# Optimization experiments

Measured on AMD Instinct MI355X. Metric: run time of the kernel, lower is better.

## Reference

```python
import jax, jax.numpy as jnp
import numpy as np

NQ = 6; DM = 128; CH = 4; SEQ = 2048; CHUNK = 16; BATCH = 128
NFP = 5 * NQ * 2   # feature params for 2 layers
NMP = 5 * NQ * 2   # mixing params for 2 layers

# ---- batched gate matrices (theta: (B,)) ----

def _rx(t):
    c = jnp.cos(t / 2).astype(jnp.complex64)
    s = (-1j * jnp.sin(t / 2)).astype(jnp.complex64)
    return jnp.stack([jnp.stack([c, s], -1), jnp.stack([s, c], -1)], -2)

def _ry(t):
    c = jnp.cos(t / 2).astype(jnp.complex64)
    s = jnp.sin(t / 2).astype(jnp.complex64)
    return jnp.stack([jnp.stack([c, -s], -1), jnp.stack([s, c], -1)], -2)

def _rz(t):
    e = jnp.exp(-1j * t.astype(jnp.complex64) / 2)
    z = jnp.zeros_like(e)
    return jnp.stack([jnp.stack([e, z], -1), jnp.stack([z, jnp.conj(e)], -1)], -2)

def _crx(t):
    B = t.shape[0]
    r = _rx(t)
    I = jnp.broadcast_to(jnp.eye(2, dtype=jnp.complex64), (B, 2, 2))
    Z = jnp.zeros((B, 2, 2), jnp.complex64)
    return jnp.concatenate([jnp.concatenate([I, Z], -1), jnp.concatenate([Z, r], -1)], -2)

# ---- batched statevector gate application; state: (B, 2, ..., 2) with axis 1+w = wire w ----

def _ap1(s, U, w):
    s = jnp.moveaxis(s, 1 + w, 1)
    sh = s.shape
    s = jnp.einsum('bij,bjr->bir', U, s.reshape(sh[0], 2, -1)).reshape(sh)
    return jnp.moveaxis(s, 1, 1 + w)

def _ap2(s, U, w0, w1):
    s = jnp.moveaxis(s, (1 + w0, 1 + w1), (1, 2))
    sh = s.shape
    s = jnp.einsum('bij,bjr->bir', U, s.reshape(sh[0], 4, -1)).reshape(sh)
    return jnp.moveaxis(s, (1, 2), (1 + w0, 1 + w1))

def _ansatz(s, p, off):
    # RX,RY,RZ on each qubit, then forward CRX ring, then backward CRX ring
    for i in range(NQ):
        s = _ap1(s, _rx(p[:, off + 3 * i]), i)
        s = _ap1(s, _ry(p[:, off + 3 * i + 1]), i)
        s = _ap1(s, _rz(p[:, off + 3 * i + 2]), i)
    off += 3 * NQ
    for i in range(NQ):
        s = _ap2(s, _crx(p[:, off]), i, (i + 1) % NQ)
        off += 1
    for i in range(NQ - 1, -1, -1):
        s = _ap2(s, _crx(p[:, off]), i, (i - 1) % NQ)
        off += 1
    return s, off

def _circuit(angles, fp, mp):
    B = angles.shape[0]
    s = jnp.zeros((B, 2 ** NQ), jnp.complex64).at[:, 0].set(1.0).reshape((B,) + (2,) * NQ)
    for i in range(NQ):                      # RY input embedding
        s = _ap1(s, _ry(angles[:, i]), i)
    off = 0
    for _ in range(2):                        # feature layers
        s, off = _ansatz(s, fp, off)
    off = 0
    for _ in range(2):                        # mixing layers
        s, off = _ansatz(s, mp, off)
    xs, ys, zs = [], [], []
    for i in range(NQ):                       # <X_i>, <Y_i>, <Z_i>
        v = jnp.moveaxis(s, 1 + i, 1).reshape(B, 2, -1)
        a, b = v[:, 0], v[:, 1]
        ab = jnp.sum(jnp.conj(a) * b, -1)
        xs.append(2 * jnp.real(ab))
        ys.append(2 * jnp.imag(ab))
        zs.append(jnp.sum(jnp.abs(a) ** 2 - jnp.abs(b) ** 2, -1))
    return jnp.stack(xs + ys + zs, 1)         # (B, 18) ordered X..Y..Z

def _ln(x, g, b, eps=1e-5):
    m = x.mean(-1, keepdims=True)
    v = ((x - m) ** 2).mean(-1, keepdims=True)
    return (x - m) / jnp.sqrt(v + eps) * g + b

def _fwd(x, conv_w, conv_b, ln1_g, ln1_b, ca1_w, ca1_b, ca2_w, ca2_b, pp_w, pp_b,
         ep_w, ep_b, op_w, op_b, ln2_g, ln2_b, sa1_w, sa1_b, sa2_w, sa2_b,
         cl1_w, cl1_b, cl2_w, cl2_b):
    B, C, S = x.shape
    h = jax.lax.conv_general_dilated(x, conv_w, (1,), [(1, 1)],
                                     dimension_numbers=('NCH', 'OIH', 'NCH')) + conv_b[None, :, None]
    h = jnp.transpose(h, (0, 2, 1))           # (B, S, D)
    h = _ln(h, ln1_g, ln1_b)
    nchunks = S // CHUNK
    h = h.reshape(B * nchunks, CHUNK, DM)
    sc = jnp.tanh(h @ ca1_w + ca1_b) @ ca2_w + ca2_b
    w = jax.nn.softmax(sc, axis=1)
    summ = jnp.sum(w * h, axis=1)             # (B*nchunks, D)
    ap = summ @ pp_w + pp_b
    fp, mp = ap[:, :NFP], ap[:, NFP:]
    ang = jnp.tanh(summ @ ep_w + ep_b) * np.pi
    q = _circuit(ang, fp, mp)                 # (B*nchunks, 18)
    cf = jax.nn.silu(_ln(q @ op_w + op_b, ln2_g, ln2_b))  # dropout = eval identity
    cf = cf.reshape(B, nchunks, DM)
    ss = jnp.tanh(cf @ sa1_w + sa1_b) @ sa2_w + sa2_b
    sw = jax.nn.softmax(ss, axis=1)
    rep = jnp.sum(sw * cf, axis=1)
    return jax.nn.silu(rep @ cl1_w + cl1_b) @ cl2_w + cl2_b

def setup_inputs() -> dict:
    key = jax.random.key(0)
    ks = jax.random.split(key, 16)
    n = lambda k, sh: (jax.random.normal(k, sh, jnp.float32) * 0.05)
    return {
        'x': jax.random.normal(ks[0], (BATCH, CH, SEQ), jnp.float32),
        'conv_w': n(ks[1], (DM, CH, 3)), 'conv_b': jnp.zeros((DM,), jnp.float32),
        'ln1_g': jnp.ones((DM,), jnp.float32), 'ln1_b': jnp.zeros((DM,), jnp.float32),
        'ca1_w': n(ks[2], (DM, DM // 4)), 'ca1_b': jnp.zeros((DM // 4,), jnp.float32),
        'ca2_w': n(ks[3], (DM // 4, 1)), 'ca2_b': jnp.zeros((1,), jnp.float32),
        'pp_w': n(ks[4], (DM, NFP + NMP)), 'pp_b': jnp.zeros((NFP + NMP,), jnp.float32),
        'ep_w': n(ks[5], (DM, NQ)), 'ep_b': jnp.zeros((NQ,), jnp.float32),
        'op_w': n(ks[6], (3 * NQ, DM)), 'op_b': jnp.zeros((DM,), jnp.float32),
        'ln2_g': jnp.ones((DM,), jnp.float32), 'ln2_b': jnp.zeros((DM,), jnp.float32),
        'sa1_w': n(ks[7], (DM, DM // 4)), 'sa1_b': jnp.zeros((DM // 4,), jnp.float32),
        'sa2_w': n(ks[8], (DM // 4, 1)), 'sa2_b': jnp.zeros((1,), jnp.float32),
        'cl1_w': n(ks[9], (DM, DM // 2)), 'cl1_b': jnp.zeros((DM // 2,), jnp.float32),
        'cl2_w': n(ks[10], (DM // 2, 2)), 'cl2_b': jnp.zeros((2,), jnp.float32),
    }

def reference(x, conv_w, conv_b, ln1_g, ln1_b, ca1_w, ca1_b, ca2_w, ca2_b, pp_w, pp_b,
              ep_w, ep_b, op_w, op_b, ln2_g, ln2_b, sa1_w, sa1_b, sa2_w, sa2_b,
              cl1_w, cl1_b, cl2_w, cl2_b):
    return _fwd(x, conv_w, conv_b, ln1_g, ln1_b, ca1_w, ca1_b, ca2_w, ca2_b, pp_w, pp_b,
                ep_w, ep_b, op_w, op_b, ln2_g, ln2_b, sa1_w, sa1_b, sa2_w, sa2_b,
                cl1_w, cl1_b, cl2_w, cl2_b)
```

## Files before the change

kernel.cpp:

```cpp
#include <hip/hip_runtime.h>
#include <math.h>


constexpr int kNQ    = 6;
constexpr int kDM    = 128;
constexpr int kCH    = 4;
constexpr int kSEQ   = 2048;
constexpr int kCHUNK = 16;
constexpr int kBATCH = 128;
constexpr int kNCH   = kSEQ / kCHUNK;
constexpr int kNP    = 120;
constexpr float kPI  = 3.14159265358979323846f;

typedef __attribute__((ext_vector_type(8))) short bf16x8;
typedef __attribute__((ext_vector_type(4))) float f32x4;

__device__ __forceinline__ float fast_tanh(float x) {
  float e = __expf(-2.f * fabsf(x));
  float r = (1.f - e) * __builtin_amdgcn_rcpf(1.f + e);
  return copysignf(r, x);
}
__device__ __forceinline__ float fast_silu(float x) {
  return x * __builtin_amdgcn_rcpf(1.f + __expf(-x));
}
// ... 62 lines not shown
}

__device__ __forceinline__ void rz_lane(float c, float sp, float* sr, float* si) {
#pragma unroll
  for (int r = 0; r < 16; ++r) {
    float ar = sr[r], ai = si[r];
    sr[r] = fmaf(c, ar, -sp * ai);
    si[r] = fmaf(c, ai,  sp * ar);
  }
}

template <int RB, int CB>
__device__ __forceinline__ void crx_reg_reg(float c, float s, float* sr, float* si) {
#pragma unroll
  for (int r0 = 0; r0 < 16; ++r0) {
    if ((r0 & RB) || !(r0 & CB)) continue;
    int r1 = r0 | RB;
    float ar = sr[r0], ai = si[r0], br = sr[r1], bi = si[r1];
    sr[r0] = fmaf(c, ar,  s * bi);  si[r0] = fmaf(c, ai, -s * br);
    sr[r1] = fmaf(c, br,  s * ai);  si[r1] = fmaf(c, bi, -s * ar);
  }
}

template <int XM, int CB>
__device__ __forceinline__ void crx_reg_lane(float c, float s, float* sr, float* si) {
#pragma unroll
  for (int r = 0; r < 16; ++r) {
    if (!(r & CB)) continue;
    float pr = qp<XM>(sr[r]), pi = qp<XM>(si[r]);
    sr[r] = fmaf(c, sr[r],  s * pi);
    si[r] = fmaf(c, si[r], -s * pr);
  }
}

template <int RB>
__device__ __forceinline__ void meas_reg(const float* sr, const float* si,
                                         float& tr, float& ti, float& zz) {
  tr = 0.f; ti = 0.f; zz = 0.f;
#pragma unroll
  for (int r0 = 0; r0 < 16; ++r0) {
    float n = fmaf(sr[r0], sr[r0], si[r0] * si[r0]);
    zz += (r0 & RB) ? -n : n;
    if (r0 & RB) continue;
    int r1 = r0 | RB;
    tr = fmaf(sr[r0], sr[r1], fmaf(si[r0], si[r1], tr));
    ti = fmaf(sr[r0], si[r1], fmaf(-si[r0], sr[r1], ti));
  }
  tr += qp<1>(tr); tr += qp<2>(tr);
  ti += qp<1>(ti); ti += qp<2>(ti);
  zz += qp<1>(zz); zz += qp<2>(zz);
}


__global__ __launch_bounds__(128) void k_pre8(
    const float* __restrict__ x,
    const float* __restrict__ conv_w, const float* __restrict__ conv_b,
    const float* __restrict__ ln1_g,  const float* __restrict__ ln1_b,
    const float* __restrict__ ca1_w,  const float* __restrict__ ca1_b,
    const float* __restrict__ ca2_w,  const float* __restrict__ ca2_b,
    const float* __restrict__ pp_w,   const float* __restrict__ pp_b,
    const float* __restrict__ ep_w,   const float* __restrict__ ep_b,
    float* __restrict__ outb, int emit_cs)
{
  constexpr int NC = 8;

  __shared__ __align__(16) float xs[kCH][NC * kCHUNK + 4];
  __shared__ __align__(16) float hbuf[kCHUNK][132];
  __shared__ __align__(16) float spart[2][16];
  __shared__ __align__(16) float wl[kCHUNK];
  __shared__ __align__(16) float sums[NC][kDM];
  __shared__ float mrow[kCHUNK], irow[kCHUNK];

  const int tid    = threadIdx.x;
  const int chunk0 = blockIdx.x * NC;
  const int b      = chunk0 >> 7;
  const int tloc   = (chunk0 & 127) * kCHUNK;
  const int d      = tid;
  const int lane   = tid & 63;
  const int wv     = tid >> 6;
  const int col    = (lane & 15) + 16 * wv;
  const int qd     = lane >> 4;

  float w12[12];
  {
    const float4* cw = (const float4*)(conv_w + d * 12);
    float4 a0 = cw[0], a1 = cw[1], a2 = cw[2];
    w12[0]=a0.x; w12[1]=a0.y; w12[2]=a0.z; w12[3]=a0.w;
    w12[4]=a1.x; w12[5]=a1.y; w12[6]=a1.z; w12[7]=a1.w;
    w12[8]=a2.x; w12[9]=a2.y; w12[10]=a2.z; w12[11]=a2.w;
  }
  float cb = conv_b[d];
  float g1 = ln1_g[d], b1 = ln1_b[d];
  float cb1 = ca1_b[col], cw2 = ca2_w[col], cb2 = ca2_b[0];

  bf16x8 bhi[4], blo[4];
#pragma unroll
  for (int ks = 0; ks < 4; ++ks)
#pragma unroll
    for (int jj = 0; jj < 8; ++jj) {
      float bvf = ca1_w[(ks * 32 + qd * 8 + jj) * 32 + col];
      unsigned bb = __float_as_uint(bvf);
      bhi[ks][jj] = (short)(bb >> 16);
      float lf = bvf - __uint_as_float(bb & 0xffff0000u);
      blo[ks][jj] = (short)(__float_as_uint(lf) >> 16);
    }

#pragma unroll
  for (int ch = 0; ch < kCH; ++ch) {
#pragma unroll
    for (int base = 0; base < 2; ++base) {
      int pos = base * 128 + tid;
      if (pos < NC * kCHUNK + 2) {
        int s = tloc - 1 + pos;
        float v = 0.f;
        if (s >= 0 && s < kSEQ) v = x[((size_t)b * kCH + ch) * kSEQ + s];
        xs[ch][pos] = v;
      }
    }
  }
  __syncthreads();

  for (int c = 0; c < NC; ++c) {
    float h[kCHUNK];
#pragma unroll
    for (int t = 0; t < kCHUNK; ++t) h[t] = cb;
#pragma unroll
    for (int ch = 0; ch < kCH; ++ch) {
      const float4* xp = (const float4*)&xs[ch][c * kCHUNK];
      float4 v0 = xp[0], v1 = xp[1], v2 = xp[2], v3 = xp[3], v4 = xp[4];
      float xr[18];
      xr[0]=v0.x; xr[1]=v0.y; xr[2]=v0.z; xr[3]=v0.w;
      xr[4]=v1.x; xr[5]=v1.y; xr[6]=v1.z; xr[7]=v1.w;
      xr[8]=v2.x; xr[9]=v2.y; xr[10]=v2.z; xr[11]=v2.w;
      xr[12]=v3.x; xr[13]=v3.y; xr[14]=v3.z; xr[15]=v3.w;
      xr[16]=v4.x; xr[17]=v4.y;
      float c0 = w12[ch*3+0], c1 = w12[ch*3+1], c2 = w12[ch*3+2];
#pragma unroll
      for (int t = 0; t < kCHUNK; ++t)
        h[t] = fmaf(xr[t], c0, fmaf(xr[t+1], c1, fmaf(xr[t+2], c2, h[t])));
    }
#pragma unroll
    for (int t = 0; t < kCHUNK; ++t) hbuf[t][d] = h[t];
    __syncthreads();

    {
      int row = tid >> 3, k = tid & 7;
      const float4* rp = (const float4*)&hbuf[row][k * 16];
      float s1 = 0.f, s2 = 0.f;
#pragma unroll
      for (int q = 0; q < 4; ++q) {
        float4 v = rp[q];
        s1 += v.x + v.y + v.z + v.w;
        s2 = fmaf(v.x,v.x,s2); s2 = fmaf(v.y,v.y,s2);
        s2 = fmaf(v.z,v.z,s2); s2 = fmaf(v.w,v.w,s2);
      }
#pragma unroll
      for (int o = 1; o < 8; o <<= 1) {
        s1 += __shfl_xor(s1, o, 64);
        s2 += __shfl_xor(s2, o, 64);
      }
      if (k == 0) {
        float m = s1 * (1.f / kDM);
        mrow[row] = m;
        irow[row] = rsqrtf(s2 * (1.f / kDM) - m * m + 1e-5f);
      }
    }
    __syncthreads();

#pragma unroll
    for (int t = 0; t < kCHUNK; ++t) {
      h[t] = fmaf((h[t] - mrow[t]) * irow[t], g1, b1);
      unsigned hb = __float_as_uint(h[t]);
      float lof = h[t] - __uint_as_float(hb & 0xffff0000u);
      unsigned pk = (hb >> 16) | (__float_as_uint(lof) & 0xffff0000u);
      ((unsigned*)&hbuf[t][0])[d] = pk;
    }
    __syncthreads();

    f32x4 acc = {0.f, 0.f, 0.f, 0.f};
    {
      const unsigned* hrow = (const unsigned*)&hbuf[lane & 15][0];
#pragma unroll
      for (int ks = 0; ks < 4; ++ks) {
        const uint4* ap = (const uint4*)(hrow + ks * 32 + qd * 8);
        uint4 w0 = ap[0], w1 = ap[1];
        bf16x8 ahi, alo;
        ahi[0] = (short)(w0.x & 0xffff); ahi[1] = (short)(w0.y & 0xffff);
        ahi[2] = (short)(w0.z & 0xffff); ahi[3] = (short)(w0.w & 0xffff);
        ahi[4] = (short)(w1.x & 0xffff); ahi[5] = (short)(w1.y & 0xffff);
        ahi[6] = (short)(w1.z & 0xffff); ahi[7] = (short)(w1.w & 0xffff);
        alo[0] = (short)(w0.x >> 16); alo[1] = (short)(w0.y >> 16);
        alo[2] = (short)(w0.z >> 16); alo[3] = (short)(w0.w >> 16);
        alo[4] = (short)(w1.x >> 16); alo[5] = (short)(w1.y >> 16);
        alo[6] = (short)(w1.z >> 16); alo[7] = (short)(w1.w >> 16);
        acc = __builtin_amdgcn_mfma_f32_16x16x32_bf16(ahi, bhi[ks], acc, 0, 0, 0);
        acc = __builtin_amdgcn_mfma_f32_16x16x32_bf16(ahi, blo[ks], acc, 0, 0, 0);
        acc = __builtin_amdgcn_mfma_f32_16x16x32_bf16(alo, bhi[ks], acc, 0, 0, 0);
      }
    }

    {
      float ev[4];
#pragma unroll
      for (int r = 0; r < 4; ++r)
        ev[r] = fast_tanh(acc[r] + cb1) * cw2;
#pragma unroll
      for (int o = 1; o < 16; o <<= 1)
#pragma unroll
        for (int r = 0; r < 4; ++r) ev[r] += __shfl_xor(ev[r], o, 64);
      if ((lane & 15) == 0)
        *(float4*)&spart[wv][qd * 4] = make_float4(ev[0], ev[1], ev[2], ev[3]);
    }
    __syncthreads();

    if (tid < 16) {
      float scl = spart[0][tid] + spart[1][tid] + cb2;
      float mx = scl;
#pragma unroll
      for (int o = 1; o < 16; o <<= 1) mx = fmaxf(mx, __shfl_xor(mx, o, 64));
      float e = __expf(scl - mx);
      float se = e;
#pragma unroll
      for (int o = 1; o < 16; o <<= 1) se += __shfl_xor(se, o, 64);
      wl[tid] = e * (1.f / se);
    }
    __syncthreads();

    {
      const float4* w4 = (const float4*)wl;
      float4 wa = w4[0], wb = w4[1], wc = w4[2], wd = w4[3];
      float acc2 = 0.f;
      acc2 = fmaf(wa.x, h[0],  acc2); acc2 = fmaf(wa.y, h[1],  acc2);
      acc2 = fmaf(wa.z, h[2],  acc2); acc2 = fmaf(wa.w, h[3],  acc2);
      acc2 = fmaf(wb.x, h[4],  acc2); acc2 = fmaf(wb.y, h[5],  acc2);
      acc2 = fmaf(wb.z, h[6],  acc2); acc2 = fmaf(wb.w, h[7],  acc2);
      acc2 = fmaf(wc.x, h[8],  acc2); acc2 = fmaf(wc.y, h[9],  acc2);
      acc2 = fmaf(wc.z, h[10], acc2); acc2 = fmaf(wc.w, h[11], acc2);
      acc2 = fmaf(wd.x, h[12], acc2); acc2 = fmaf(wd.y, h[13], acc2);
      acc2 = fmaf(wd.z, h[14], acc2); acc2 = fmaf(wd.w, h[15], acc2);
      sums[c][d] = acc2;
    }
  }
  __syncthreads();

  if (tid < kNP + kNQ) {
    const bool isep = (tid >= kNP);
    const int  jj   = tid - kNP;
    const float* wp = isep ? (ep_w + jj) : (pp_w + tid);
    const int  ws   = isep ? kNQ : kNP;
    const int  ws2  = ws * 2, ws3 = ws * 3, ws4 = ws * 4;
    float bias = isep ? ep_b[jj] : pp_b[tid];
    float accp[NC];
#pragma unroll
    for (int c = 0; c < NC; ++c) accp[c] = bias;
#pragma unroll 4
    for (int q4 = 0; q4 < 32; ++q4) {
      float w0 = wp[0], w1 = wp[ws], w2 = wp[ws2], w3 = wp[ws3];
      wp += ws4;
#pragma unroll
      for (int c = 0; c < NC; ++c) {
        float4 s = *(const float4*)&sums[c][q4 * 4];
        accp[c] = fmaf(s.x, w0, fmaf(s.y, w1, fmaf(s.z, w2, fmaf(s.w, w3, accp[c]))));
      }
    }
    const int slot = isep ? jj : (6 + tid);
#pragma unroll
    for (int c = 0; c < NC; ++c) {
      int chunkg = chunk0 + c;
      float ha = isep ? (0.5f * fast_tanh(accp[c]) * kPI) : (0.5f * accp[c]);
      if (emit_cs) {
        ((float2*)(outb + (size_t)chunkg * 256))[slot] =
            make_float2(__cosf(ha), __sinf(ha));
      } else {
        outb[(size_t)chunkg * 126 + slot] = ha;
      }
    }
  }
}


constexpr int kCsStride = 260;

__global__ __launch_bounds__(64) void k_circ_cs(const float* __restrict__ csA,
                                                float* __restrict__ qv_g)
{
  __shared__ __align__(16) float lds[16 * kCsStride];

  const int lane  = threadIdx.x;
  const int c     = lane >> 2;
  const int l     = lane & 3;
  const int chunk = blockIdx.x * 16 + c;
  const int b0 = (l >> 1) & 1;
  const int b1 = l & 1;

  {
    const float4* src = (const float4*)(csA + (size_t)blockIdx.x * 16 * 256);
#pragma unroll
    for (int i = 0; i < 16; ++i) {
      float4 v = src[i * 64 + lane];
      *(float4*)&lds[i * kCsStride + lane * 4] = v;
    }
  }
  __syncthreads();

  const float2* cp = (const float2*)&lds[c * kCsStride];

  float sr[16], si[16];
#pragma unroll
  for (int r = 0; r < 16; ++r) { sr[r] = 0.f; si[r] = 0.f; }
  sr[0] = (l == 0) ? 1.f : 0.f;

  {
    float2 q0 = cp[0], q1 = cp[1], q2 = cp[2], q3 = cp[3], q4 = cp[4], q5 = cp[5];
    ry_lane<2>(q0.x, b0 ? q0.y : -q0.y, sr, si);
    ry_lane<1>(q1.x, b1 ? q1.y : -q1.y, sr, si);
    ry_reg<8>(q2.x, q2.y, sr, si);
    ry_reg<4>(q3.x, q3.y, sr, si);
    ry_reg<2>(q4.x, q4.y, sr, si);
    ry_reg<1>(q5.x, q5.y, sr, si);
  }

  for (int a = 0; a < 4; ++a) {
    const float2* pb = cp + 6 + a * 30;
    float2 t;
    t = pb[0];  rx_lane<2>(t.x, t.y, sr, si);
    t = pb[1];  ry_lane<2>(t.x, b0 ? t.y : -t.y, sr, si);
    t = pb[2];  rz_lane   (t.x, b0 ? t.y : -t.y, sr, si);
    t = pb[3];  rx_lane<1>(t.x, t.y, sr, si);
    t = pb[4];  ry_lane<1>(t.x, b1 ? t.y : -t.y, sr, si);
    t = pb[5];  rz_lane   (t.x, b1 ? t.y : -t.y, sr, si);
    t = pb[6];  rx_reg<8>(t.x, t.y, sr, si);
    t = pb[7];  ry_reg<8>(t.x, t.y, sr, si);
    t = pb[8];  rz_reg<8>(t.x, t.y, sr, si);
    t = pb[9];  rx_reg<4>(t.x, t.y, sr, si);
    t = pb[10]; ry_reg<4>(t.x, t.y, sr, si);
    t = pb[11]; rz_reg<4>(t.x, t.y, sr, si);
    t = pb[12]; rx_reg<2>(t.x, t.y, sr, si);
    t = pb[13]; ry_reg<2>(t.x, t.y, sr, si);
    t = pb[14]; rz_reg<2>(t.x, t.y, sr, si);
    t = pb[15]; rx_reg<1>(t.x, t.y, sr, si);
    t = pb[16]; ry_reg<1>(t.x, t.y, sr, si);
    t = pb[17]; rz_reg<1>(t.x, t.y, sr, si);
    t = pb[18]; { float c2 = b0 ? t.x : 1.f, s2 = b0 ? t.y : 0.f; rx_lane<1>(c2, s2, sr, si); }
    t = pb[19]; { float c2 = b1 ? t.x : 1.f, s2 = b1 ? t.y : 0.f; rx_reg<8>(c2, s2, sr, si); }
    t = pb[20]; crx_reg_reg<4, 8>(t.x, t.y, sr, si);
    t = pb[21]; crx_reg_reg<2, 4>(t.x, t.y, sr, si);
    t = pb[22]; crx_reg_reg<1, 2>(t.x, t.y, sr, si);
    t = pb[23]; crx_reg_lane<2, 1>(t.x, t.y, sr, si);
    t = pb[24]; crx_reg_reg<2, 1>(t.x, t.y, sr, si);
    t = pb[25]; crx_reg_reg<4, 2>(t.x, t.y, sr, si);
    t = pb[26]; crx_reg_reg<8, 4>(t.x, t.y, sr, si);
    t = pb[27]; crx_reg_lane<1, 8>(t.x, t.y, sr, si);
    t = pb[28]; { float c2 = b1 ? t.x : 1.f, s2 = b1 ? t.y : 0.f; rx_lane<2>(c2, s2, sr, si); }
    t = pb[29]; { float c2 = b0 ? t.x : 1.f, s2 = b0 ? t.y : 0.f; rx_reg<1>(c2, s2, sr, si); }
  }

  float res[18];
  {
    float tr = 0.f, ti = 0.f, zz = 0.f;
#pragma unroll
    for (int r = 0; r < 16; ++r) {
      float pr = qp<2>(sr[r]), pi = qp<2>(si[r]);
      tr = fmaf(sr[r], pr, fmaf(si[r], pi, tr));
      ti = fmaf(sr[r], pi, fmaf(-si[r], pr, ti));
      zz = fmaf(sr[r], sr[r], fmaf(si[r], si[r], zz));
    }
    tr = b0 ? 0.f : tr;  ti = b0 ? 0.f : ti;  zz = b0 ? -zz : zz;
    tr += qp<1>(tr); tr += qp<2>(tr);
    ti += qp<1>(ti); ti += qp<2>(ti);
    zz += qp<1>(zz); zz += qp<2>(zz);
    res[0] = 2.f * tr; res[6] = 2.f * ti; res[12] = zz;
  }
  {
    float tr = 0.f, ti = 0.f, zz = 0.f;
#pragma unroll
    for (int r = 0; r < 16; ++r) {
      float pr = qp<1>(sr[r]), pi = qp<1>(si[r]);
      tr = fmaf(sr[r], pr, fmaf(si[r], pi, tr));
      ti = fmaf(sr[r], pi, fmaf(-si[r], pr, ti));
      zz = fmaf(sr[r], sr[r], fmaf(si[r], si[r], zz));
    }
    tr = b1 ? 0.f : tr;  ti = b1 ? 0.f : ti;  zz = b1 ? -zz : zz;
    tr += qp<1>(tr); tr += qp<2>(tr);
    ti += qp<1>(ti); ti += qp<2>(ti);
    zz += qp<1>(zz); zz += qp<2>(zz);
    res[1] = 2.f * tr; res[7] = 2.f * ti; res[13] = zz;
  }
  {
    float tr, ti, zz;
    meas_reg<8>(sr, si, tr, ti, zz); res[2] = 2.f*tr; res[8]  = 2.f*ti; res[14] = zz;
    meas_reg<4>(sr, si, tr, ti, zz); res[3] = 2.f*tr; res[9]  = 2.f*ti; res[15] = zz;
    meas_reg<2>(sr, si, tr, ti, zz); res[4] = 2.f*tr; res[10] = 2.f*ti; res[16] = zz;
    meas_reg<1>(sr, si, tr, ti, zz); res[5] = 2.f*tr; res[11] = 2.f*ti; res[17] = zz;
  }
  if (l == 0) {
    float* qo = qv_g + (size_t)chunk * 18;
#pragma unroll
    for (int k = 0; k < 18; ++k) qo[k] = res[k];
  }
}


__global__ __launch_bounds__(64) void k_circ(const float* __restrict__ csb_g,
                                             float* __restrict__ qv_g)
{
  const int lane  = threadIdx.x;
  const int c     = lane >> 2;
  const int l     = lane & 3;
  const int chunk = blockIdx.x * 16 + c;
  const float* cp = csb_g + (size_t)chunk * 126;
  const int b0 = (l >> 1) & 1;
  const int b1 = l & 1;

  float sr[16], si[16];
#pragma unroll
  for (int r = 0; r < 16; ++r) { sr[r] = 0.f; si[r] = 0.f; }
  sr[0] = (l == 0) ? 1.f : 0.f;

  {
    float gc[6], gs[6];
#pragma unroll
    for (int g = 0; g < 6; ++g) { float th = cp[g]; gc[g] = __cosf(th); gs[g] = __sinf(th); }
    ry_lane<2>(gc[0], b0 ? gs[0] : -gs[0], sr, si);
    ry_lane<1>(gc[1], b1 ? gs[1] : -gs[1], sr, si);
    ry_reg<8>(gc[2], gs[2], sr, si);
    ry_reg<4>(gc[3], gs[3], sr, si);
    ry_reg<2>(gc[4], gs[4], sr, si);
    ry_reg<1>(gc[5], gs[5], sr, si);
  }

  for (int a = 0; a < 4; ++a) {
    const float* pb = cp + 6 + a * 30;
    float gc[30], gs[30];
#pragma unroll
    for (int g = 0; g < 30; ++g) { float th = pb[g]; gc[g] = __cosf(th); gs[g] = __sinf(th); }
    rx_lane<2>(gc[0], gs[0], sr, si);
    ry_lane<2>(gc[1], b0 ? gs[1] : -gs[1], sr, si);
    rz_lane   (gc[2], b0 ? gs[2] : -gs[2], sr, si);
    rx_lane<1>(gc[3], gs[3], sr, si);
    ry_lane<1>(gc[4], b1 ? gs[4] : -gs[4], sr, si);
    rz_lane   (gc[5], b1 ? gs[5] : -gs[5], sr, si);
    rx_reg<8>(gc[6],  gs[6],  sr, si);  ry_reg<8>(gc[7],  gs[7],  sr, si);  rz_reg<8>(gc[8],  gs[8],  sr, si);
    rx_reg<4>(gc[9],  gs[9],  sr, si);  ry_reg<4>(gc[10], gs[10], sr, si);  rz_reg<4>(gc[11], gs[11], sr, si);
    rx_reg<2>(gc[12], gs[12], sr, si);  ry_reg<2>(gc[13], gs[13], sr, si);  rz_reg<2>(gc[14], gs[14], sr, si);
    rx_reg<1>(gc[15], gs[15], sr, si);  ry_reg<1>(gc[16], gs[16], sr, si);  rz_reg<1>(gc[17], gs[17], sr, si);
    { float c2 = b0 ? gc[18] : 1.f, s2 = b0 ? gs[18] : 0.f; rx_lane<1>(c2, s2, sr, si); }
    { float c2 = b1 ? gc[19] : 1.f, s2 = b1 ? gs[19] : 0.f; rx_reg<8>(c2, s2, sr, si); }
// ... 434 lines not shown
  int tid = threadIdx.x, wid = tid >> 6, lane = tid & 63;
  int pair = blockIdx.x * 4 + wid;
  int j = lane & 31, hh = lane >> 5;
  const float4* row = (const float4*)(cf + (size_t)pair*kDM + hh*64);
  const float* wp = sa1_w + (hh*64)*32 + j;
  float acc = 0.f;
#pragma unroll
  for (int q = 0; q < 16; ++q) {
    float4 v = row[q];
    acc = fmaf(v.x,wp[(q*4+0)*32],acc); acc = fmaf(v.y,wp[(q*4+1)*32],acc);
    acc = fmaf(v.z,wp[(q*4+2)*32],acc); acc = fmaf(v.w,wp[(q*4+3)*32],acc);
  }
  acc += __shfl_xor(acc, 32, 64);
  float hv = fast_tanh(acc + sa1_b[j]);
  float v = hv * sa2_w[j];
#pragma unroll
  for (int o = 16; o; o >>= 1) v += __shfl_xor(v, o, 64);
  if (lane == 0) scl[pair] = v + sa2_b[0];
}


extern "C" void kernel_launch(void* const* d_in, const int* in_sizes, int n_in,
                              void* d_out, int out_size, void* d_ws, size_t ws_size,
                              hipStream_t stream) {
  const float* x      = (const float*)d_in[0];
  const float* conv_w = (const float*)d_in[1];
  const float* conv_b = (const float*)d_in[2];
  const float* ln1_g  = (const float*)d_in[3];
  const float* ln1_b  = (const float*)d_in[4];
  const float* ca1_w  = (const float*)d_in[5];
  const float* ca1_b  = (const float*)d_in[6];
  const float* ca2_w  = (const float*)d_in[7];
  const float* ca2_b  = (const float*)d_in[8];
  const float* pp_w   = (const float*)d_in[9];
  const float* pp_b   = (const float*)d_in[10];
  const float* ep_w   = (const float*)d_in[11];
  const float* ep_b   = (const float*)d_in[12];
  const float* op_w   = (const float*)d_in[13];
  const float* op_b   = (const float*)d_in[14];
  const float* ln2_g  = (const float*)d_in[15];
  const float* ln2_b  = (const float*)d_in[16];
  const float* sa1_w  = (const float*)d_in[17];
  const float* sa1_b  = (const float*)d_in[18];
  const float* sa2_w  = (const float*)d_in[19];
  const float* sa2_b  = (const float*)d_in[20];
  const float* cl1_w  = (const float*)d_in[21];
  const float* cl1_b  = (const float*)d_in[22];
  const float* cl2_w  = (const float*)d_in[23];
  const float* cl2_b  = (const float*)d_in[24];
  float* out = (float*)d_out;

  const size_t nch   = (size_t)kBATCH * kNCH;
  const size_t fCS   = nch * 256;
  const size_t need1 = (fCS + nch * 18 + nch) * sizeof(float);
  const size_t fA    = nch * kDM;
  const size_t need2 = (fA + nch * 18 + nch) * sizeof(float);

  if (ws_size >= need1) {
    float* csA   = (float*)d_ws;
    float* cf    = csA;
    float* qv_g  = csA + fCS;
    float* sclb  = qv_g + nch * 18;
    k_pre8<<<(kBATCH * kNCH) / 8, 128, 0, stream>>>(
        x, conv_w, conv_b, ln1_g, ln1_b, ca1_w, ca1_b, ca2_w, ca2_b,
        pp_w, pp_b, ep_w, ep_b, csA, 1);
    k_circ_cs<<<(kBATCH * kNCH) / 16, 64, 0, stream>>>(csA, qv_g);
    k_post<<<kBATCH * kNCH, 128, 0, stream>>>(
        qv_g, op_w, op_b, ln2_g, ln2_b, sa1_w, sa1_b, sa2_w, sa2_b, cf, sclb);
    k_pool_cf<<<kBATCH, 512, 0, stream>>>(
        cf, sclb, cl1_w, cl1_b, cl2_w, cl2_b, out);
  } else if (ws_size >= need2) {
    float* A     = (float*)d_ws;
    float* qv_g  = A + fA;
    float* sclb  = qv_g + nch * 18;
    k_pre8<<<(kBATCH * kNCH) / 8, 128, 0, stream>>>(
        x, conv_w, conv_b, ln1_g, ln1_b, ca1_w, ca1_b, ca2_w, ca2_b,
        pp_w, pp_b, ep_w, ep_b, A, 0);
    k_circ<<<(kBATCH * kNCH) / 16, 64, 0, stream>>>(A, qv_g);
    k_post<<<kBATCH * kNCH, 128, 0, stream>>>(
        qv_g, op_w, op_b, ln2_g, ln2_b, sa1_w, sa1_b, sa2_w, sa2_b, A, sclb);
    k_pool_cf<<<kBATCH, 512, 0, stream>>>(
        A, sclb, cl1_w, cl1_b, cl2_w, cl2_b, out);
  } else {
    float* cf   = (float*)d_ws;
    float* sclb = cf + nch * kDM;
    k_chunk_fb<<<kBATCH * kNCH, 128, 0, stream>>>(
        x, conv_w, conv_b, ln1_g, ln1_b, ca1_w, ca1_b, ca2_w, ca2_b,
        pp_w, pp_b, ep_w, ep_b, op_w, op_b, ln2_g, ln2_b, cf);
    k_scl_fb<<<(kBATCH * kNCH) / 4, 256, 0, stream>>>(cf, sa1_w, sa1_b, sa2_w, sa2_b, sclb);
    k_pool_cf<<<kBATCH, 512, 0, stream>>>(cf, sclb, cl1_w, cl1_b, cl2_w, cl2_b, out);
  }
}
```

Before: 208.2 us.

## Fuse quantum circuit simulation with post-processing into one kernel

Adds a k_circ_post kernel that runs the circuit simulation for 16 chunks in one wavefront and then, in the same 256-thread block, does the output projection, LayerNorm, SiLU and attention-score work that k_post did. This removes a launch and the global round-trip of the 18-value measurement vectors. The circuit body moves into a shared device function. The trade-off is that 3 of the 4 waves sit idle during the circuit phase, and the post stage now runs sequentially over 8 chunks per slot with block barriers instead of one block per chunk.

Measured after the change: 192.0 us (median of 2 runs). -7.8%, faster.

```diff
diff --git a/kernel.cpp b/kernel.cpp
--- a/kernel.cpp
+++ b/kernel.cpp
@@ -138,259 +138,9 @@
 }
 
 
-__global__ __launch_bounds__(128) void k_pre8(
-    const float* __restrict__ x,
-    const float* __restrict__ conv_w, const float* __restrict__ conv_b,
-    const float* __restrict__ ln1_g,  const float* __restrict__ ln1_b,
-    const float* __restrict__ ca1_w,  const float* __restrict__ ca1_b,
-    const float* __restrict__ ca2_w,  const float* __restrict__ ca2_b,
-    const float* __restrict__ pp_w,   const float* __restrict__ pp_b,
-    const float* __restrict__ ep_w,   const float* __restrict__ ep_b,
-    float* __restrict__ outb, int emit_cs)
-{
-  constexpr int NC = 8;
-
-  __shared__ __align__(16) float xs[kCH][NC * kCHUNK + 4];
-  __shared__ __align__(16) float hbuf[kCHUNK][132];
-  __shared__ __align__(16) float spart[2][16];
-  __shared__ __align__(16) float wl[kCHUNK];
-  __shared__ __align__(16) float sums[NC][kDM];
-  __shared__ float mrow[kCHUNK], irow[kCHUNK];
-
-  const int tid    = threadIdx.x;
-  const int chunk0 = blockIdx.x * NC;
-  const int b      = chunk0 >> 7;
-  const int tloc   = (chunk0 & 127) * kCHUNK;
-  const int d      = tid;
-  const int lane   = tid & 63;
-  const int wv     = tid >> 6;
-  const int col    = (lane & 15) + 16 * wv;
-  const int qd     = lane >> 4;
-
-  float w12[12];
-  {
-    const float4* cw = (const float4*)(conv_w + d * 12);
-    float4 a0 = cw[0], a1 = cw[1], a2 = cw[2];
-    w12[0]=a0.x; w12[1]=a0.y; w12[2]=a0.z; w12[3]=a0.w;
-    w12[4]=a1.x; w12[5]=a1.y; w12[6]=a1.z; w12[7]=a1.w;
-    w12[8]=a2.x; w12[9]=a2.y; w12[10]=a2.z; w12[11]=a2.w;
-  }
-  float cb = conv_b[d];
-  float g1 = ln1_g[d], b1 = ln1_b[d];
-  float cb1 = ca1_b[col], cw2 = ca2_w[col], cb2 = ca2_b[0];
-
-  bf16x8 bhi[4], blo[4];
-#pragma unroll
-  for (int ks = 0; ks < 4; ++ks)
-#pragma unroll
-    for (int jj = 0; jj < 8; ++jj) {
-      float bvf = ca1_w[(ks * 32 + qd * 8 + jj) * 32 + col];
-      unsigned bb = __float_as_uint(bvf);
-      bhi[ks][jj] = (short)(bb >> 16);
-      float lf = bvf - __uint_as_float(bb & 0xffff0000u);
-      blo[ks][jj] = (short)(__float_as_uint(lf) >> 16);
-    }
-
-#pragma unroll
-  for (int ch = 0; ch < kCH; ++ch) {
-#pragma unroll
-    for (int base = 0; base < 2; ++base) {
-      int pos = base * 128 + tid;
-      if (pos < NC * kCHUNK + 2) {
-        int s = tloc - 1 + pos;
-        float v = 0.f;
-        if (s >= 0 && s < kSEQ) v = x[((size_t)b * kCH + ch) * kSEQ + s];
-        xs[ch][pos] = v;
-      }
-    }
-  }
-  __syncthreads();
-
-  for (int c = 0; c < NC; ++c) {
-    float h[kCHUNK];
-#pragma unroll
-    for (int t = 0; t < kCHUNK; ++t) h[t] = cb;
-#pragma unroll
-    for (int ch = 0; ch < kCH; ++ch) {
-      const float4* xp = (const float4*)&xs[ch][c * kCHUNK];
-      float4 v0 = xp[0], v1 = xp[1], v2 = xp[2], v3 = xp[3], v4 = xp[4];
-      float xr[18];
-      xr[0]=v0.x; xr[1]=v0.y; xr[2]=v0.z; xr[3]=v0.w;
-      xr[4]=v1.x; xr[5]=v1.y; xr[6]=v1.z; xr[7]=v1.w;
-      xr[8]=v2.x; xr[9]=v2.y; xr[10]=v2.z; xr[11]=v2.w;
-      xr[12]=v3.x; xr[13]=v3.y; xr[14]=v3.z; xr[15]=v3.w;
-      xr[16]=v4.x; xr[17]=v4.y;
-      float c0 = w12[ch*3+0], c1 = w12[ch*3+1], c2 = w12[ch*3+2];
-#pragma unroll
-      for (int t = 0; t < kCHUNK; ++t)
-        h[t] = fmaf(xr[t], c0, fmaf(xr[t+1], c1, fmaf(xr[t+2], c2, h[t])));
-    }
-#pragma unroll
-    for (int t = 0; t < kCHUNK; ++t) hbuf[t][d] = h[t];
-    __syncthreads();
-
-    {
-      int row = tid >> 3, k = tid & 7;
-      const float4* rp = (const float4*)&hbuf[row][k * 16];
-      float s1 = 0.f, s2 = 0.f;
-#pragma unroll
-      for (int q = 0; q < 4; ++q) {
-        float4 v = rp[q];
-        s1 += v.x + v.y + v.z + v.w;
-        s2 = fmaf(v.x,v.x,s2); s2 = fmaf(v.y,v.y,s2);
-        s2 = fmaf(v.z,v.z,s2); s2 = fmaf(v.w,v.w,s2);
-      }
-#pragma unroll
-      for (int o = 1; o < 8; o <<= 1) {
-        s1 += __shfl_xor(s1, o, 64);
-        s2 += __shfl_xor(s2, o, 64);
-      }
-      if (k == 0) {
-        float m = s1 * (1.f / kDM);
-        mrow[row] = m;
-        irow[row] = rsqrtf(s2 * (1.f / kDM) - m * m + 1e-5f);
-      }
-    }
-    __syncthreads();
-
-#pragma unroll
-    for (int t = 0; t < kCHUNK; ++t) {
-      h[t] = fmaf((h[t] - mrow[t]) * irow[t], g1, b1);
-      unsigned hb = __float_as_uint(h[t]);
-      float lof = h[t] - __uint_as_float(hb & 0xffff0000u);
-      unsigned pk = (hb >> 16) | (__float_as_uint(lof) & 0xffff0000u);
-      ((unsigned*)&hbuf[t][0])[d] = pk;
-    }
-    __syncthreads();
-
-    f32x4 acc = {0.f, 0.f, 0.f, 0.f};
-    {
-      const unsigned* hrow = (const unsigned*)&hbuf[lane & 15][0];
-#pragma unroll
-      for (int ks = 0; ks < 4; ++ks) {
-        const uint4* ap = (const uint4*)(hrow + ks * 32 + qd * 8);
-        uint4 w0 = ap[0], w1 = ap[1];
-        bf16x8 ahi, alo;
-        ahi[0] = (short)(w0.x & 0xffff); ahi[1] = (short)(w0.y & 0xffff);
-        ahi[2] = (short)(w0.z & 0xffff); ahi[3] = (short)(w0.w & 0xffff);
-        ahi[4] = (short)(w1.x & 0xffff); ahi[5] = (short)(w1.y & 0xffff);
-        ahi[6] = (short)(w1.z & 0xffff); ahi[7] = (short)(w1.w & 0xffff);
-        alo[0] = (short)(w0.x >> 16); alo[1] = (short)(w0.y >> 16);
-        alo[2] = (short)(w0.z >> 16); alo[3] = (short)(w0.w >> 16);
-        alo[4] = (short)(w1.x >> 16); alo[5] = (short)(w1.y >> 16);
-        alo[6] = (short)(w1.z >> 16); alo[7] = (short)(w1.w >> 16);
-        acc = __builtin_amdgcn_mfma_f32_16x16x32_bf16(ahi, bhi[ks], acc, 0, 0, 0);
-        acc = __builtin_amdgcn_mfma_f32_16x16x32_bf16(ahi, blo[ks], acc, 0, 0, 0);
-        acc = __builtin_amdgcn_mfma_f32_16x16x32_bf16(alo, bhi[ks], acc, 0, 0, 0);
-      }
-    }
-
-    {
-      float ev[4];
-#pragma unroll
-      for (int r = 0; r < 4; ++r)
-        ev[r] = fast_tanh(acc[r] + cb1) * cw2;
-#pragma unroll
-      for (int o = 1; o < 16; o <<= 1)
-#pragma unroll
-        for (int r = 0; r < 4; ++r) ev[r] += __shfl_xor(ev[r], o, 64);
-      if ((lane & 15) == 0)
-        *(float4*)&spart[wv][qd * 4] = make_float4(ev[0], ev[1], ev[2], ev[3]);
-    }
-    __syncthreads();
-
-    if (tid < 16) {
-      float scl = spart[0][tid] + spart[1][tid] + cb2;
-      float mx = scl;
-#pragma unroll
-      for (int o = 1; o < 16; o <<= 1) mx = fmaxf(mx, __shfl_xor(mx, o, 64));
-      float e = __expf(scl - mx);
-      float se = e;
-#pragma unroll
-      for (int o = 1; o < 16; o <<= 1) se += __shfl_xor(se, o, 64);
-      wl[tid] = e * (1.f / se);
-    }
-    __syncthreads();
-
-    {
-      const float4* w4 = (const float4*)wl;
-      float4 wa = w4[0], wb = w4[1], wc = w4[2], wd = w4[3];
-      float acc2 = 0.f;
-      acc2 = fmaf(wa.x, h[0],  acc2); acc2 = fmaf(wa.y, h[1],  acc2);
-      acc2 = fmaf(wa.z, h[2],  acc2); acc2 = fmaf(wa.w, h[3],  acc2);
-      acc2 = fmaf(wb.x, h[4],  acc2); acc2 = fmaf(wb.y, h[5],  acc2);
-      acc2 = fmaf(wb.z, h[6],  acc2); acc2 = fmaf(wb.w, h[7],  acc2);
-      acc2 = fmaf(wc.x, h[8],  acc2); acc2 = fmaf(wc.y, h[9],  acc2);
-      acc2 = fmaf(wc.z, h[10], acc2); acc2 = fmaf(wc.w, h[11], acc2);
-      acc2 = fmaf(wd.x, h[12], acc2); acc2 = fmaf(wd.y, h[13], acc2);
-      acc2 = fmaf(wd.z, h[14], acc2); acc2 = fmaf(wd.w, h[15], acc2);
-      sums[c][d] = acc2;
-    }
-  }
-  __syncthreads();
-
-  if (tid < kNP + kNQ) {
-    const bool isep = (tid >= kNP);
-    const int  jj   = tid - kNP;
-    const float* wp = isep ? (ep_w + jj) : (pp_w + tid);
-    const int  ws   = isep ? kNQ : kNP;
-    const int  ws2  = ws * 2, ws3 = ws * 3, ws4 = ws * 4;
-    float bias = isep ? ep_b[jj] : pp_b[tid];
-    float accp[NC];
-#pragma unroll
-    for (int c = 0; c < NC; ++c) accp[c] = bias;
-#pragma unroll 4
-    for (int q4 = 0; q4 < 32; ++q4) {
-      float w0 = wp[0], w1 = wp[ws], w2 = wp[ws2], w3 = wp[ws3];
-      wp += ws4;
-#pragma unroll
-      for (int c = 0; c < NC; ++c) {
-        float4 s = *(const float4*)&sums[c][q4 * 4];
-        accp[c] = fmaf(s.x, w0, fmaf(s.y, w1, fmaf(s.z, w2, fmaf(s.w, w3, accp[c]))));
-      }
-    }
-    const int slot = isep ? jj : (6 + tid);
-#pragma unroll
-    for (int c = 0; c < NC; ++c) {
-      int chunkg = chunk0 + c;
-      float ha = isep ? (0.5f * fast_tanh(accp[c]) * kPI) : (0.5f * accp[c]);
-      if (emit_cs) {
-        ((float2*)(outb + (size_t)chunkg * 256))[slot] =
-            make_float2(__cosf(ha), __sinf(ha));
-      } else {
-        outb[(size_t)chunkg * 126 + slot] = ha;
-      }
-    }
-  }
-}
-
-
-constexpr int kCsStride = 260;
-
-__global__ __launch_bounds__(64) void k_circ_cs(const float* __restrict__ csA,
-                                                float* __restrict__ qv_g)
-{
-  __shared__ __align__(16) float lds[16 * kCsStride];
-
-  const int lane  = threadIdx.x;
-  const int c     = lane >> 2;
-  const int l     = lane & 3;
-  const int chunk = blockIdx.x * 16 + c;
-  const int b0 = (l >> 1) & 1;
-  const int b1 = l & 1;
-
-  {
-    const float4* src = (const float4*)(csA + (size_t)blockIdx.x * 16 * 256);
-#pragma unroll
-    for (int i = 0; i < 16; ++i) {
-      float4 v = src[i * 64 + lane];
-      *(float4*)&lds[i * kCsStride + lane * 4] = v;
-    }
-  }
-  __syncthreads();
-
-  const float2* cp = (const float2*)&lds[c * kCsStride];
-
+__device__ __forceinline__ void circ_from_cs(const float2* __restrict__ cp,
+                                             int l, int b0, int b1,
+                                             float* __restrict__ res) {
   float sr[16], si[16];
 #pragma unroll
   for (int r = 0; r < 16; ++r) { sr[r] = 0.f; si[r] = 0.f; }
@@ -441,7 +191,6 @@
     t = pb[29]; { float c2 = b0 ? t.x : 1.f, s2 = b0 ? t.y : 0.f; rx_reg<1>(c2, s2, sr, si); }
   }
 
-  float res[18];
   {
     float tr = 0.f, ti = 0.f, zz = 0.f;
 #pragma unroll
@@ -479,6 +228,368 @@
     meas_reg<2>(sr, si, tr, ti, zz); res[4] = 2.f*tr; res[10] = 2.f*ti; res[16] = zz;
     meas_reg<1>(sr, si, tr, ti, zz); res[5] = 2.f*tr; res[11] = 2.f*ti; res[17] = zz;
   }
+}
+
+
+__global__ __launch_bounds__(128) void k_pre8(
+    const float* __restrict__ x,
+    const float* __restrict__ conv_w, const float* __restrict__ conv_b,
+    const float* __restrict__ ln1_g,  const float* __restrict__ ln1_b,
+    const float* __restrict__ ca1_w,  const float* __restrict__ ca1_b,
+    const float* __restrict__ ca2_w,  const float* __restrict__ ca2_b,
+    const float* __restrict__ pp_w,   const float* __restrict__ pp_b,
+    const float* __restrict__ ep_w,   const float* __restrict__ ep_b,
+    float* __restrict__ outb, int emit_cs)
+{
+  constexpr int NC = 8;
+
+  __shared__ __align__(16) float xs[kCH][NC * kCHUNK + 4];
+  __shared__ __align__(16) float hbuf[kCHUNK][132];
+  __shared__ __align__(16) float spart[2][16];
+  __shared__ __align__(16) float wl[kCHUNK];
+  __shared__ __align__(16) float sums[NC][kDM];
+  __shared__ float mrow[kCHUNK], irow[kCHUNK];
+
+  const int tid    = threadIdx.x;
+  const int chunk0 = blockIdx.x * NC;
+  const int b      = chunk0 >> 7;
+  const int tloc   = (chunk0 & 127) * kCHUNK;
+  const int d      = tid;
+  const int lane   = tid & 63;
+  const int wv     = tid >> 6;
+  const int col    = (lane & 15) + 16 * wv;
+  const int qd     = lane >> 4;
+
+  float w12[12];
+  {
+    const float4* cw = (const float4*)(conv_w + d * 12);
+    float4 a0 = cw[0], a1 = cw[1], a2 = cw[2];
+    w12[0]=a0.x; w12[1]=a0.y; w12[2]=a0.z; w12[3]=a0.w;
+    w12[4]=a1.x; w12[5]=a1.y; w12[6]=a1.z; w12[7]=a1.w;
+    w12[8]=a2.x; w12[9]=a2.y; w12[10]=a2.z; w12[11]=a2.w;
+  }
+  float cb = conv_b[d];
+  float g1 = ln1_g[d], b1 = ln1_b[d];
+  float cb1 = ca1_b[col], cw2 = ca2_w[col], cb2 = ca2_b[0];
+
+  bf16x8 bhi[4], blo[4];
+#pragma unroll
+  for (int ks = 0; ks < 4; ++ks)
+#pragma unroll
+    for (int jj = 0; jj < 8; ++jj) {
+      float bvf = ca1_w[(ks * 32 + qd * 8 + jj) * 32 + col];
+      unsigned bb = __float_as_uint(bvf);
+      bhi[ks][jj] = (short)(bb >> 16);
+      float lf = bvf - __uint_as_float(bb & 0xffff0000u);
+      blo[ks][jj] = (short)(__float_as_uint(lf) >> 16);
+    }
+
+#pragma unroll
+  for (int ch = 0; ch < kCH; ++ch) {
+#pragma unroll
+    for (int base = 0; base < 2; ++base) {
+      int pos = base * 128 + tid;
+      if (pos < NC * kCHUNK + 2) {
+        int s = tloc - 1 + pos;
+        float v = 0.f;
+        if (s >= 0 && s < kSEQ) v = x[((size_t)b * kCH + ch) * kSEQ + s];
+        xs[ch][pos] = v;
+      }
+    }
+  }
+  __syncthreads();
+
+  for (int c = 0; c < NC; ++c) {
+    float h[kCHUNK];
+#pragma unroll
+    for (int t = 0; t < kCHUNK; ++t) h[t] = cb;
+#pragma unroll
+    for (int ch = 0; ch < kCH; ++ch) {
+      const float4* xp = (const float4*)&xs[ch][c * kCHUNK];
+      float4 v0 = xp[0], v1 = xp[1], v2 = xp[2], v3 = xp[3], v4 = xp[4];
+      float xr[18];
+      xr[0]=v0.x; xr[1]=v0.y; xr[2]=v0.z; xr[3]=v0.w;
+      xr[4]=v1.x; xr[5]=v1.y; xr[6]=v1.z; xr[7]=v1.w;
+      xr[8]=v2.x; xr[9]=v2.y; xr[10]=v2.z; xr[11]=v2.w;
+      xr[12]=v3.x; xr[13]=v3.y; xr[14]=v3.z; xr[15]=v3.w;
+      xr[16]=v4.x; xr[17]=v4.y;
+      float c0 = w12[ch*3+0], c1 = w12[ch*3+1], c2 = w12[ch*3+2];
+#pragma unroll
+      for (int t = 0; t < kCHUNK; ++t)
+        h[t] = fmaf(xr[t], c0, fmaf(xr[t+1], c1, fmaf(xr[t+2], c2, h[t])));
+    }
+#pragma unroll
+    for (int t = 0; t < kCHUNK; ++t) hbuf[t][d] = h[t];
+    __syncthreads();
+
+    {
+      int row = tid >> 3, k = tid & 7;
+      const float4* rp = (const float4*)&hbuf[row][k * 16];
+      float s1 = 0.f, s2 = 0.f;
+#pragma unroll
+      for (int q = 0; q < 4; ++q) {
+        float4 v = rp[q];
+        s1 += v.x + v.y + v.z + v.w;
+        s2 = fmaf(v.x,v.x,s2); s2 = fmaf(v.y,v.y,s2);
+        s2 = fmaf(v.z,v.z,s2); s2 = fmaf(v.w,v.w,s2);
+      }
+#pragma unroll
+      for (int o = 1; o < 8; o <<= 1) {
+        s1 += __shfl_xor(s1, o, 64);
+        s2 += __shfl_xor(s2, o, 64);
+      }
+      if (k == 0) {
+        float m = s1 * (1.f / kDM);
+        mrow[row] = m;
+        irow[row] = rsqrtf(s2 * (1.f / kDM) - m * m + 1e-5f);
+      }
+    }
+    __syncthreads();
+
+#pragma unroll
+    for (int t = 0; t < kCHUNK; ++t) {
+      h[t] = fmaf((h[t] - mrow[t]) * irow[t], g1, b1);
+      unsigned hb = __float_as_uint(h[t]);
+      float lof = h[t] - __uint_as_float(hb & 0xffff0000u);
+      unsigned pk = (hb >> 16) | (__float_as_uint(lof) & 0xffff0000u);
+      ((unsigned*)&hbuf[t][0])[d] = pk;
+    }
+    __syncthreads();
+
+    f32x4 acc = {0.f, 0.f, 0.f, 0.f};
+    {
+      const unsigned* hrow = (const unsigned*)&hbuf[lane & 15][0];
+#pragma unroll
+      for (int ks = 0; ks < 4; ++ks) {
+        const uint4* ap = (const uint4*)(hrow + ks * 32 + qd * 8);
+        uint4 w0 = ap[0], w1 = ap[1];
+        bf16x8 ahi, alo;
+        ahi[0] = (short)(w0.x & 0xffff); ahi[1] = (short)(w0.y & 0xffff);
+        ahi[2] = (short)(w0.z & 0xffff); ahi[3] = (short)(w0.w & 0xffff);
+        ahi[4] = (short)(w1.x & 0xffff); ahi[5] = (short)(w1.y & 0xffff);
+        ahi[6] = (short)(w1.z & 0xffff); ahi[7] = (short)(w1.w & 0xffff);
+        alo[0] = (short)(w0.x >> 16); alo[1] = (short)(w0.y >> 16);
+        alo[2] = (short)(w0.z >> 16); alo[3] = (short)(w0.w >> 16);
+        alo[4] = (short)(w1.x >> 16); alo[5] = (short)(w1.y >> 16);
+        alo[6] = (short)(w1.z >> 16); alo[7] = (short)(w1.w >> 16);
+        acc = __builtin_amdgcn_mfma_f32_16x16x32_bf16(ahi, bhi[ks], acc, 0, 0, 0);
+        acc = __builtin_amdgcn_mfma_f32_16x16x32_bf16(ahi, blo[ks], acc, 0, 0, 0);
+        acc = __builtin_amdgcn_mfma_f32_16x16x32_bf16(alo, bhi[ks], acc, 0, 0, 0);
+      }
+    }
+
+    {
+      float ev[4];
+#pragma unroll
+      for (int r = 0; r < 4; ++r)
+        ev[r] = fast_tanh(acc[r] + cb1) * cw2;
+#pragma unroll
+      for (int o = 1; o < 16; o <<= 1)
+#pragma unroll
+        for (int r = 0; r < 4; ++r) ev[r] += __shfl_xor(ev[r], o, 64);
+      if ((lane & 15) == 0)
+        *(float4*)&spart[wv][qd * 4] = make_float4(ev[0], ev[1], ev[2], ev[3]);
+    }
+    __syncthreads();
+
+    if (tid < 16) {
+      float scl = spart[0][tid] + spart[1][tid] + cb2;
+      float mx = scl;
+#pragma unroll
+      for (int o = 1; o < 16; o <<= 1) mx = fmaxf(mx, __shfl_xor(mx, o, 64));
+      float e = __expf(scl - mx);
+      float se = e;
+#pragma unroll
+      for (int o = 1; o < 16; o <<= 1) se += __shfl_xor(se, o, 64);
+      wl[tid] = e * (1.f / se);
+    }
+    __syncthreads();
+
+    {
+      const float4* w4 = (const float4*)wl;
+      float4 wa = w4[0], wb = w4[1], wc = w4[2], wd = w4[3];
+      float acc2 = 0.f;
+      acc2 = fmaf(wa.x, h[0],  acc2); acc2 = fmaf(wa.y, h[1],  acc2);
+      acc2 = fmaf(wa.z, h[2],  acc2); acc2 = fmaf(wa.w, h[3],  acc2);
+      acc2 = fmaf(wb.x, h[4],  acc2); acc2 = fmaf(wb.y, h[5],  acc2);
+      acc2 = fmaf(wb.z, h[6],  acc2); acc2 = fmaf(wb.w, h[7],  acc2);
+      acc2 = fmaf(wc.x, h[8],  acc2); acc2 = fmaf(wc.y, h[9],  acc2);
+      acc2 = fmaf(wc.z, h[10], acc2); acc2 = fmaf(wc.w, h[11], acc2);
+      acc2 = fmaf(wd.x, h[12], acc2); acc2 = fmaf(wd.y, h[13], acc2);
+      acc2 = fmaf(wd.z, h[14], acc2); acc2 = fmaf(wd.w, h[15], acc2);
+      sums[c][d] = acc2;
+    }
+  }
+  __syncthreads();
+
+  if (tid < kNP + kNQ) {
+    const bool isep = (tid >= kNP);
+    const int  jj   = tid - kNP;
+    const float* wp = isep ? (ep_w + jj) : (pp_w + tid);
+    const int  ws   = isep ? kNQ : kNP;
+    const int  ws2  = ws * 2, ws3 = ws * 3, ws4 = ws * 4;
+    float bias = isep ? ep_b[jj] : pp_b[tid];
+    float accp[NC];
+#pragma unroll
+    for (int c = 0; c < NC; ++c) accp[c] = bias;
+#pragma unroll 4
+    for (int q4 = 0; q4 < 32; ++q4) {
+      float w0 = wp[0], w1 = wp[ws], w2 = wp[ws2], w3 = wp[ws3];
+      wp += ws4;
+#pragma unroll
+      for (int c = 0; c < NC; ++c) {
+        float4 s = *(const float4*)&sums[c][q4 * 4];
+        accp[c] = fmaf(s.x, w0, fmaf(s.y, w1, fmaf(s.z, w2, fmaf(s.w, w3, accp[c]))));
+      }
+    }
+    const int slot = isep ? jj : (6 + tid);
+#pragma unroll
+    for (int c = 0; c < NC; ++c) {
+      int chunkg = chunk0 + c;
+      float ha = isep ? (0.5f * fast_tanh(accp[c]) * kPI) : (0.5f * accp[c]);
+      if (emit_cs) {
+        ((float2*)(outb + (size_t)chunkg * 256))[slot] =
+            make_float2(__cosf(ha), __sinf(ha));
+      } else {
+        outb[(size_t)chunkg * 126 + slot] = ha;
+      }
+    }
+  }
+}
+
+
+constexpr int kCsStride = 260;
+
+__global__ __launch_bounds__(256) void k_circ_post(
+    const float* __restrict__ csA,
+    const float* __restrict__ op_w, const float* __restrict__ op_b,
+    const float* __restrict__ ln2_g, const float* __restrict__ ln2_b,
+    const float* __restrict__ sa1_w, const float* __restrict__ sa1_b,
+    const float* __restrict__ sa2_w, const float* __restrict__ sa2_b,
+    float* __restrict__ cf, float* __restrict__ sclb)
+{
+  __shared__ __align__(16) float lds[16 * kCsStride];
+  __shared__ __align__(16) float qvs[16][19];
+  __shared__ __align__(16) float cfs[2][132];
+  __shared__ float part1[2][32];
+  __shared__ float redA[2][2], redB[2][2];
+
+  const int tid = threadIdx.x;
+
+  {
+    const float4* src = (const float4*)(csA + (size_t)blockIdx.x * 16 * 256);
+#pragma unroll
+    for (int jq = 0; jq < 4; ++jq) {
+      int idx = jq * 256 + tid;
+      int ic = idx >> 6, ln = idx & 63;
+      *(float4*)&lds[ic * kCsStride + ln * 4] = src[idx];
+    }
+  }
+  __syncthreads();
+
+  if (tid < 64) {
+    const int c  = tid >> 2;
+    const int l  = tid & 3;
+    const int b0 = (l >> 1) & 1;
+    const int b1 = l & 1;
+    float res[18];
+    circ_from_cs((const float2*)&lds[c * kCsStride], l, b0, b1, res);
+    if (l == 0) {
+#pragma unroll
+      for (int k = 0; k < 18; ++k) qvs[c][k] = res[k];
+    }
+  }
+
+  const int d    = tid & 127;
+  const int slot = tid >> 7;
+  const int j    = d & 31;
+  const int sub  = d >> 5;
+  float ow[18];
+#pragma unroll
+  for (int k = 0; k < 18; ++k) ow[k] = op_w[k * kDM + d];
+  float ob = op_b[d], g2 = ln2_g[d], b2 = ln2_b[d];
+  float wreg[32];
+  {
+    const float* wp2 = sa1_w + (sub * 32) * 32 + j;
+#pragma unroll
+    for (int k = 0; k < 32; ++k) wreg[k] = wp2[k * 32];
+  }
+  float s1b = sa1_b[j], s2w = sa2_w[j], s2b = sa2_b[0];
+  __syncthreads();
+
+  for (int i = 0; i < 8; ++i) {
+    const int c      = slot * 8 + i;
+    const int chunkg = blockIdx.x * 16 + c;
+
+    float qv[18];
+#pragma unroll
+    for (int k = 0; k < 18; ++k) qv[k] = qvs[c][k];
+    float acc = ob;
+#pragma unroll
+    for (int k = 0; k < 18; ++k) acc = fmaf(qv[k], ow[k], acc);
+
+    float v = acc, v2 = acc * acc;
+#pragma unroll
+    for (int o = 32; o; o >>= 1) { v += __shfl_xor(v, o, 64); v2 += __shfl_xor(v2, o, 64); }
+    if ((d & 63) == 0) { redA[slot][d >> 6] = v; redB[slot][d >> 6] = v2; }
+    __syncthreads();
+    float ss1 = redA[slot][0] + redA[slot][1];
+    float ss2 = redB[slot][0] + redB[slot][1];
+    float m = ss1 * (1.f / kDM);
+    float var = ss2 * (1.f / kDM) - m * m;
+    float xn = fmaf((acc - m) * rsqrtf(var + 1e-5f), g2, b2);
+    float cfv = fast_silu(xn);
+    cf[(size_t)chunkg * kDM + d] = cfv;
+    cfs[slot][d] = cfv;
+    __syncthreads();
+
+    float acc2 = 0.f;
+#pragma unroll
+    for (int q = 0; q < 8; ++q) {
+      float4 hv = *(const float4*)&cfs[slot][sub * 32 + q * 4];
+      acc2 = fmaf(hv.x, wreg[q*4+0], acc2);
+      acc2 = fmaf(hv.y, wreg[q*4+1], acc2);
+      acc2 = fmaf(hv.z, wreg[q*4+2], acc2);
+      acc2 = fmaf(hv.w, wreg[q*4+3], acc2);
+    }
+    acc2 += __shfl_xor(acc2, 32, 64);
+    if (sub == 2) part1[slot][j] = acc2;
+    __syncthreads();
+    if (d < 32) {
+      float hv = fast_tanh(acc2 + part1[slot][j] + s1b) * s2w;
+#pragma unroll
+      for (int o = 16; o; o >>= 1) hv += __shfl_xor(hv, o, 64);
+      if (j == 0) sclb[chunkg] = hv + s2b;
+    }
+  }
+}
+
+
+__global__ __launch_bounds__(64) void k_circ_cs(const float* __restrict__ csA,
+                                                float* __restrict__ qv_g)
+{
+  __shared__ __align__(16) float lds[16 * kCsStride];
+
+  const int lane  = threadIdx.x;
+  const int c     = lane >> 2;
+  const int l     = lane & 3;
+  const int chunk = blockIdx.x * 16 + c;
+  const int b0 = (l >> 1) & 1;
+  const int b1 = l & 1;
+
+  {
+    const float4* src = (const float4*)(csA + (size_t)blockIdx.x * 16 * 256);
+#pragma unroll
+    for (int i = 0; i < 16; ++i) {
+      float4 v = src[i * 64 + lane];
+      *(float4*)&lds[i * kCsStride + lane * 4] = v;
+    }
+  }
+  __syncthreads();
+
+  float res[18];
+  circ_from_cs((const float2*)&lds[c * kCsStride], l, b0, b1, res);
+
   if (l == 0) {
     float* qo = qv_g + (size_t)chunk * 18;
 #pragma unroll
@@ -1019,11 +1130,23 @@
 
   const size_t nch   = (size_t)kBATCH * kNCH;
   const size_t fCS   = nch * 256;
+  const size_t fA    = nch * kDM;
+  const size_t need0 = (fCS + fA + nch) * sizeof(float);
   const size_t need1 = (fCS + nch * 18 + nch) * sizeof(float);
-  const size_t fA    = nch * kDM;
   const size_t need2 = (fA + nch * 18 + nch) * sizeof(float);
 
-  if (ws_size >= need1) {
+  if (ws_size >= need0) {
+    float* csA   = (float*)d_ws;
+    float* cf2   = csA + fCS;
+    float* sclb  = cf2 + fA;
+    k_pre8<<<(kBATCH * kNCH) / 8, 128, 0, stream>>>(
+        x, conv_w, conv_b, ln1_g, ln1_b, ca1_w, ca1_b, ca2_w, ca2_b,
+        pp_w, pp_b, ep_w, ep_b, csA, 1);
+    k_circ_post<<<(kBATCH * kNCH) / 16, 256, 0, stream>>>(
+        csA, op_w, op_b, ln2_g, ln2_b, sa1_w, sa1_b, sa2_w, sa2_b, cf2, sclb);
+    k_pool_cf<<<kBATCH, 512, 0, stream>>>(
+        cf2, sclb, cl1_w, cl1_b, cl2_w, cl2_b, out);
+  } else if (ws_size >= need1) {
     float* csA   = (float*)d_ws;
     float* cf    = csA;
     float* qv_g  = csA + fCS;
```
